# Kernel tuning notes

Measured on AMD Instinct MI355X. Metric: run time of the kernel, lower is better.

## Reference

```python
import jax, jax.numpy as jnp
import numpy as np

THRESHOLD = 0.3

def setup_inputs() -> dict:
    key = jax.random.key(0)
    ks = jax.random.split(key, 8)
    B, T, N, d = 4, 32, 1024, 2
    hd, od, hs, osz = 64, 64, 128, 2
    p = lambda k, sh: jax.random.normal(k, sh, jnp.float32) * 0.1
    return {
        "points": jax.random.uniform(ks[0], (B, T, N, d), jnp.float32),
        "W1": p(ks[1], (hd, d)),   "b1": jnp.zeros((hd,), jnp.float32),
        "W2": p(ks[2], (od, hd)),  "b2": jnp.zeros((od,), jnp.float32),
        "Wg": p(ks[3], (hd, od)),  "bg": jnp.zeros((hd,), jnp.float32),
        "Wih": p(ks[4], (3 * hs, hd)), "Whh": p(ks[5], (3 * hs, hs)),
        "bih": jnp.zeros((3 * hs,), jnp.float32), "bhh": jnp.zeros((3 * hs,), jnp.float32),
        "Wf": p(ks[6], (osz, hs)), "bf": jnp.zeros((osz,), jnp.float32),
    }

def _gcn_step(pts, W1, b1, W2, b2, Wg, bg):
    # pts: [N, d]. Torch detaches node features & adjacency (no grad to points).
    pts = jax.lax.stop_gradient(pts)
    dist = jnp.linalg.norm(pts[:, None, :] - pts[None, :, :], axis=2)  # [N,N]
    A = (dist < THRESHOLD).astype(pts.dtype)
    dinv = 1.0 / jnp.sqrt(A.sum(axis=1))          # rowsum >= 1 (self-loop)
    An = A * dinv[:, None] * dinv[None, :]        # D^{-1/2} A D^{-1/2}
    x = jax.nn.relu((An @ pts) @ W1.T + b1)       # [N, hd]
    x = jax.nn.relu((An @ x) @ W2.T + b2)         # [N, od]
    return x.mean(axis=0) @ Wg.T + bg             # [hd]

def reference(points, W1, b1, W2, b2, Wg, bg, Wih, Whh, bih, bhh, Wf, bf):
    # GCN per (batch, time): [B, T, hd]
    gcn = jax.vmap(jax.vmap(lambda p: _gcn_step(p, W1, b1, W2, b2, Wg, bg)))(points)
    H = Whh.shape[1]

    def gru_step(h, x):  # torch GRU gate order: r, z, n
        gi = x @ Wih.T + bih
        gh = h @ Whh.T + bhh
        ir, iz, inn = jnp.split(gi, 3)
        hr, hz, hn = jnp.split(gh, 3)
        r = jax.nn.sigmoid(ir + hr)
        z = jax.nn.sigmoid(iz + hz)
        n = jnp.tanh(inn + r * hn)
        h_new = (1.0 - z) * n + z * h
        return h_new, h_new

    h0 = jnp.zeros((H,), points.dtype)
    run = lambda xs: jax.lax.scan(gru_step, h0, xs)[1]   # [T, H]
    hs = jax.vmap(run)(gcn)                              # [B, T, H]
    y = hs @ Wf.T + bf                                   # [B, T, out]
    # torch: per-element gru_out.mean(dim=1, keepdim=True) on [1,T,out] -> [1,1,out], stacked -> [B,1,1,out]
    return y.mean(axis=1, keepdims=True)[:, :, None, :]
```

## Files before the change

kernel.cpp:

```cpp
#include <hip/hip_runtime.h>
#include <hip/hip_bf16.h>
#include <math.h>

#define N_PTS 1024
#define BT    128
typedef unsigned int u32;
typedef __attribute__((ext_vector_type(8))) short short8_t;
typedef __attribute__((ext_vector_type(4))) float f32x4;

__device__ __forceinline__ float bfi(u32 bits16) {
    union { u32 u; float f; } v; v.u = bits16 << 16; return v.f;
}
__device__ __forceinline__ unsigned short f2bf(float f) {
    union { float f; u32 u; } v; v.f = f;
    return (unsigned short)((v.u + 0x7FFFu + ((v.u >> 16) & 1u)) >> 16);
}
__device__ __forceinline__ float ldf(const void* p, int i, bool bf) {
    return bf ? bfi(((const unsigned short*)p)[i]) : ((const float*)p)[i];
}
__device__ __forceinline__ float2 ldp(const void* pbase, int j, bool bf) {
    if (bf) {
        u32 w = ((const u32*)pbase)[j];
        return make_float2(bfi(w & 0xFFFFu), bfi(w >> 16));
    }
    return ((const float2*)pbase)[j];
}
__device__ __forceinline__ bool detect_bf16(const void* pts, int tid, int* s_flag) {
    if (tid < 64) {
        u32 w = ((const u32*)pts)[tid];
        float v = bfi(w & 0xFFFFu);
        bool ok = (v >= 0.0f) && (v <= 1.0f);
        unsigned long long m = __ballot(ok);
        if (tid == 0) *s_flag = (m == 0xFFFFFFFFFFFFFFFFull) ? 1 : 0;
    }
    __syncthreads();
    return *s_flag != 0;
}
__device__ __forceinline__ bool is_nb(float px, float py, float qx, float qy) {
    float dx = px - qx, dy = py - qy;
    float d2 = __fadd_rn(__fmul_rn(dx, dx), __fmul_rn(dy, dy));
    return d2 < 0.09f;
}
__device__ __forceinline__ const void* pts_base(const void* pts, int bt, bool bf) {
    return bf ? (const void*)((const unsigned short*)pts + (size_t)bt * N_PTS * 2)
              : (const void*)((const float*)pts + (size_t)bt * N_PTS * 2);
}
__device__ __forceinline__ void gload16(const u32* g, u32* l) {
    __builtin_amdgcn_global_load_lds((const __attribute__((address_space(1))) u32*)g,
                                     (__attribute__((address_space(3))) u32*)l, 16, 0, 0);
}
__device__ __forceinline__ float rdlane(float v, int i) {
    return __int_as_float(__builtin_amdgcn_readlane(__float_as_int(v), i));
}

__global__ __launch_bounds__(256) void k1_bm(const void* __restrict__ pts,
                                             float* __restrict__ dinv,
                                             float* __restrict__ gsum,
                                             u32* __restrict__ bm) {
    int blk = blockIdx.x, tid = threadIdx.x;
    int bt = blk >> 2, q = blk & 3;
    __shared__ float2 sp[N_PTS];
    __shared__ int s_flag;
    bool bf = detect_bf16(pts, tid, &s_flag);
    const void* pb = pts_base(pts, bt, bf);
    for (int j = tid; j < N_PTS; j += 256) sp[j] = ldp(pb, j, bf);
    if (blk < 32) gsum[blk * 256 + tid] = 0.0f;
    __syncthreads();
    int i = q * 256 + tid;
    float px = sp[i].x, py = sp[i].y;
    const float4* sp4 = (const float4*)sp;
    u32* bmrow = bm + (size_t)bt * 32768 + i;
    int cnt = 0;
    for (int c = 0; c < 32; c++) {
        u32 m = 0;
#pragma unroll
        for (int h = 0; h < 8; h++) {
            float4 s01 = sp4[c * 16 + 2 * h], s23 = sp4[c * 16 + 2 * h + 1];
            if (is_nb(px, py, s01.x, s01.y)) m |= 1u << (4 * h);
            if (is_nb(px, py, s01.z, s01.w)) m |= 1u << (4 * h + 1);
            if (is_nb(px, py, s23.x, s23.y)) m |= 1u << (4 * h + 2);
            if (is_nb(px, py, s23.z, s23.w)) m |= 1u << (4 * h + 3);
        }
        bmrow[c * 1024] = m;
        cnt += __popc(m);
    }
    dinv[bt * N_PTS + i] = 1.0f / sqrtf((float)cnt);
}

__global__ __launch_bounds__(256) void k2_x1v(const void* __restrict__ pts,
                                              const void* __restrict__ W1,
                                              const void* __restrict__ b1,
                                              const float* __restrict__ dinv,
                                              const u32* __restrict__ bm,
                                              u32* __restrict__ x1vB) {
    int blk = blockIdx.x, tid = threadIdx.x;
    int bt = blk >> 2, q = blk & 3;
    __shared__ float2 sud[N_PTS];
    __shared__ float2 sax[256];
    __shared__ float  sdl[256];
    __shared__ int s_flag;
    bool bf = detect_bf16(pts, tid, &s_flag);
    const void* pb = pts_base(pts, bt, bf);
    for (int j = tid; j < N_PTS; j += 256) {
        float2 p = ldp(pb, j, bf);
        float d = dinv[bt * N_PTS + j];
        sud[j] = make_float2(d * p.x, d * p.y);
    }
    __syncthreads();
    int i = q * 256 + tid;
    float ax = 0.f, ay = 0.f;
    const u32* bmr = bm + (size_t)bt * 32768 + i;
    for (int c = 0; c < 32; c++) {
        u32 m = bmr[c * 1024];
        const float4* uv = (const float4*)sud + c * 16;
#pragma unroll
        for (int h = 0; h < 16; h++) {
            float4 v = uv[h];
            bool b0 = (m >> (2 * h)) & 1u, b1_ = (m >> (2 * h + 1)) & 1u;
            ax += b0 ? v.x : 0.0f;  ay += b0 ? v.y : 0.0f;
            ax += b1_ ? v.z : 0.0f; ay += b1_ ? v.w : 0.0f;
        }
    }
    float di = dinv[bt * N_PTS + i];
    sax[tid] = make_float2(ax * di, ay * di);
    sdl[tid] = di;
    __syncthreads();
    int ch = tid & 63, wq = tid >> 6;
    float w0 = ldf(W1, 2 * ch, bf), w1v = ldf(W1, 2 * ch + 1, bf), bb = ldf(b1, ch, bf);
    for (int tt = 0; tt < 4; tt++) {
        u32 ow[8];
#pragma unroll
        for (int k2i = 0; k2i < 8; k2i++) {
            int lj = tt * 64 + wq * 16 + 2 * k2i;
            float2 a0 = sax[lj], a1 = sax[lj + 1];
            float v0 = sdl[lj]     * fmaxf(fmaf(w0, a0.x, fmaf(w1v, a0.y, bb)), 0.0f);
            float v1 = sdl[lj + 1] * fmaxf(fmaf(w0, a1.x, fmaf(w1v, a1.y, bb)), 0.0f);
            ow[k2i] = (u32)f2bf(v0) | ((u32)f2bf(v1) << 16);
        }
        u32* dst = x1vB + ((size_t)(bt * 16 + q * 4 + tt) * 64 + ch) * 36 + wq * 8;
        *(uint4*)dst = make_uint4(ow[0], ow[1], ow[2], ow[3]);
        *(uint4*)(dst + 4) = make_uint4(ow[4], ow[5], ow[6], ow[7]);
    }
}

__global__ __launch_bounds__(256) void k3_mfma(const void* __restrict__ pts,
                                               const void* __restrict__ W2,
                                               const void* __restrict__ b2,
                                               const float* __restrict__ dinv,
                                               const u32* __restrict__ bm,
                                               const u32* __restrict__ x1vB,
                                               float* __restrict__ gsum) {
    __shared__ u32 pool[15424];
    __shared__ int s_flag;
    float* poolf = (float*)pool;
    int tid = threadIdx.x, lane = tid & 63, w = tid >> 6;
    int l15 = lane & 15, quad = lane >> 4;
    int blk = blockIdx.x, bt = blk & 127, rowblk = blk >> 7;
    bool bf = detect_bf16(pts, tid, &s_flag);

    const u32* xg = x1vB + (size_t)bt * 36864;
    for (int it = w; it < 9; it += 4)
        gload16(xg + it * 256 + lane * 4, pool + 8192 + it * 256 + lane * 4);

    const u32* bg_ = bm + (size_t)bt * 32768 + rowblk * 256;
    for (int idx = tid; idx < 8192; idx += 256) {
        int c = idx >> 8, r = idx & 255;
        pool[idx] = bg_[c * 1024 + r];
    }
    unsigned short* W2B = (unsigned short*)(pool + 12800);
    for (int idx = tid; idx < 4096; idx += 256) {
        int o = idx >> 6, c = idx & 63;
        W2B[o * 72 + c] = f2bf(ldf(W2, idx, bf));
    }
    if (tid < 256) poolf[15104 + tid] = dinv[bt * N_PTS + rowblk * 256 + tid];
    if (tid < 64)  poolf[15360 + tid] = ldf(b2, tid, bf);

    f32x4 acc[4][4];
#pragma unroll
    for (int rf = 0; rf < 4; rf++)
#pragma unroll
        for (int nb = 0; nb < 4; nb++)
#pragma unroll
            for (int r = 0; r < 4; r++) acc[rf][nb][r] = 0.0f;

    for (int t = 0; t < 16; t++) {
        __syncthreads();
        if (t + 1 < 16) {
            u32* dst = pool + ((t & 1) ? 8192 : 10496);
            const u32* src = xg + (t + 1) * 2304;
            for (int it = w; it < 9; it += 4)
                gload16(src + it * 256 + lane * 4, dst + it * 256 + lane * 4);
        }
        const unsigned short* xf = (const unsigned short*)(pool + ((t & 1) ? 10496 : 8192));
#pragma unroll
        for (int ks = 0; ks < 2; ks++) {
            short8_t bq[4];
#pragma unroll
            for (int rf = 0; rf < 4; rf++) {
                u32 mw = pool[(2 * t + ks) * 256 + w * 64 + rf * 16 + l15];
                u32 by = (mw >> (quad * 8)) & 0xFFu;
                short8_t v;
#pragma unroll
                for (int i2 = 0; i2 < 8; i2++)
                    v[i2] = (by & (1u << i2)) ? (short)0x3F80 : (short)0;
                bq[rf] = v;
            }
#pragma unroll
            for (int nb = 0; nb < 4; nb++) {
                short8_t af = *(const short8_t*)(xf + (nb * 16 + l15) * 72 + ks * 32 + quad * 8);
#pragma unroll
                for (int rf = 0; rf < 4; rf++)
                    acc[rf][nb] = __builtin_amdgcn_mfma_f32_16x16x32_bf16(af, bq[rf], acc[rf][nb], 0, 0, 0);
            }
        }
    }
    __syncthreads();

    u32* dump = pool;
#pragma unroll
    for (int rf = 0; rf < 4; rf++) {
        int rn = w * 64 + rf * 16 + l15;
        float di = poolf[15104 + rn];
#pragma unroll
        for (int nb = 0; nb < 4; nb++) {
            u32 lo = (u32)f2bf(acc[rf][nb][0] * di) | ((u32)f2bf(acc[rf][nb][1] * di) << 16);
            u32 hi = (u32)f2bf(acc[rf][nb][2] * di) | ((u32)f2bf(acc[rf][nb][3] * di) << 16);
            u32* dst = dump + rn * 36 + nb * 8 + quad * 2;
            dst[0] = lo; dst[1] = hi;
        }
    }
    __syncthreads();
    f32x4 xacc[4][4];
#pragma unroll
    for (int ob = 0; ob < 4; ob++)
#pragma unroll
        for (int rf = 0; rf < 4; rf++)
#pragma unroll
            for (int r = 0; r < 4; r++) xacc[ob][rf][r] = 0.0f;
#pragma unroll
    for (int ks2 = 0; ks2 < 2; ks2++) {
        short8_t b2f[4];
#pragma unroll
        for (int rf = 0; rf < 4; rf++)
            b2f[rf] = *(const short8_t*)((const unsigned short*)dump +
                        (w * 64 + rf * 16 + l15) * 72 + ks2 * 32 + quad * 8);
#pragma unroll
        for (int ob = 0; ob < 4; ob++) {
            short8_t a2 = *(const short8_t*)(W2B + (ob * 16 + l15) * 72 + ks2 * 32 + quad * 8);
#pragma unroll
            for (int rf = 0; rf < 4; rf++)
                xacc[ob][rf] = __builtin_amdgcn_mfma_f32_16x16x32_bf16(a2, b2f[rf], xacc[ob][rf], 0, 0, 0);
        }
    }
#pragma unroll
    for (int ob = 0; ob < 4; ob++) {
#pragma unroll
        for (int r = 0; r < 4; r++) {
            int o = ob * 16 + quad * 4 + r;
            float bb = poolf[15360 + o];
            float s = 0.0f;
#pragma unroll
            for (int rf = 0; rf < 4; rf++) s += fmaxf(xacc[ob][rf][r] + bb, 0.0f);
            s += __shfl_down(s, 8, 16);
            s += __shfl_down(s, 4, 16);
            s += __shfl_down(s, 2, 16);
            s += __shfl_down(s, 1, 16);
            if (l15 == 0) atomicAdd(&gsum[bt * 64 + o], s);
        }
    }
}

__global__ __launch_bounds__(768, 1) void k4_all(const void* __restrict__ pts,
                                                 const void* __restrict__ Wg,
                                                 const void* __restrict__ bg,
                                                 const void* __restrict__ Wih,
                                                 const void* __restrict__ Whh,
                                                 const void* __restrict__ bih,
                                                 const void* __restrict__ bhh,
                                                 const void* __restrict__ Wf,
                                                 const void* __restrict__ bf_,
                                                 const float* __restrict__ gsum,
                                                 float* __restrict__ out) {
    int b = blockIdx.x, tid = threadIdx.x;
    __shared__ float s_gi[32 * 384];
    __shared__ float sWgT[64 * 65];
    __shared__ float s_gm[2048];
    __shared__ float s_x[2048];
    __shared__ float s_part[768];
    __shared__ float s_h[128];
    __shared__ int s_flag;
    bool bf = detect_bf16(pts, tid, &s_flag);
    for (int idx = tid; idx < 4096; idx += 768) {
        int o = idx >> 6, k = idx & 63;
        sWgT[k * 65 + o] = ldf(Wg, idx, bf);
    }
    for (int idx = tid; idx < 2048; idx += 768)
        s_gm[idx] = gsum[(size_t)b * 2048 + idx] * (1.0f / 1024.0f);
    if (tid < 128) s_h[tid] = 0.0f;
    __syncthreads();
    for (int idx = tid; idx < 2048; idx += 768) {
        int t = idx >> 6, c = idx & 63;
        float s0 = ldf(bg, c, bf), s1 = 0.f, s2 = 0.f, s3 = 0.f;
        const float* gm = s_gm + t * 64;
#pragma unroll
        for (int k = 0; k < 64; k += 4) {
            s0 = fmaf(sWgT[k * 65 + c],       gm[k],     s0);
            s1 = fmaf(sWgT[(k + 1) * 65 + c], gm[k + 1], s1);
            s2 = fmaf(sWgT[(k + 2) * 65 + c], gm[k + 2], s2);
            s3 = fmaf(sWgT[(k + 3) * 65 + c], gm[k + 3], s3);
        }
        s_x[idx] = (s0 + s1) + (s2 + s3);
    }
    __syncthreads();
    int hi = (tid >= 384) ? 1 : 0;
    int r = tid - hi * 384;
    int lane = tid & 63;
    {
        float wv[64];
        if (bf) {
#pragma unroll
            for (int k = 0; k < 64; k++) wv[k] = bfi(((const unsigned short*)Wih)[r * 64 + k]);
        } else {
            const float4* wr = (const float4*)Wih + r * 16;
#pragma unroll
            for (int qq = 0; qq < 16; qq++) {
                float4 v = wr[qq];
                wv[4*qq] = v.x; wv[4*qq+1] = v.y; wv[4*qq+2] = v.z; wv[4*qq+3] = v.w;
            }
        }
        float br = ldf(bih, r, bf);
        for (int t = hi; t < 32; t += 2) {
            float xv = s_x[t * 64 + lane];
            float s0 = br, s1 = 0.f, s2 = 0.f, s3 = 0.f;
#pragma unroll
            for (int k = 0; k < 64; k += 4) {
                s0 = fmaf(wv[k],     rdlane(xv, k),     s0);
                s1 = fmaf(wv[k + 1], rdlane(xv, k + 1), s1);
                s2 = fmaf(wv[k + 2], rdlane(xv, k + 2), s2);
                s3 = fmaf(wv[k + 3], rdlane(xv, k + 3), s3);
            }
            s_gi[t * 384 + r] = (s0 + s1) + (s2 + s3);
        }
    }
    float wh2[64];
    {
        int koff = hi * 64;
        if (bf) {
#pragma unroll
            for (int k = 0; k < 64; k++)
                wh2[k] = bfi(((const unsigned short*)Whh)[r * 128 + koff + k]);
        } else {
            const float4* wr = (const float4*)Whh + (r * 128 + koff) / 4;
#pragma unroll
            for (int qq = 0; qq < 16; qq++) {
                float4 v = wr[qq];
                wh2[4*qq] = v.x; wh2[4*qq+1] = v.y; wh2[4*qq+2] = v.z; wh2[4*qq+3] = v.w;
            }
        }
    }
    float bhr = hi ? 0.0f : ldf(bhh, r, bf);
    float h_reg = 0.0f, hsum = 0.0f;
    __syncthreads();

    for (int t = 0; t < 32; t++) {
        float hval = s_h[hi * 64 + lane];
        float s0 = bhr, s1 = 0.f, s2 = 0.f, s3 = 0.f;
#pragma unroll
        for (int k = 0; k < 64; k += 4) {
            s0 = fmaf(wh2[k],     rdlane(hval, k),     s0);
            s1 = fmaf(wh2[k + 1], rdlane(hval, k + 1), s1);
            s2 = fmaf(wh2[k + 2], rdlane(hval, k + 2), s2);
            s3 = fmaf(wh2[k + 3], rdlane(hval, k + 3), s3);
        }
        s_part[tid] = (s0 + s1) + (s2 + s3);
        __syncthreads();
        if (tid < 128) {
            int c = tid;
            float gr = s_gi[t * 384 + c]       + s_part[c]       + s_part[384 + c];
            float gz = s_gi[t * 384 + 128 + c] + s_part[128 + c] + s_part[512 + c];
            float gn = s_gi[t * 384 + 256 + c];
            float hn = s_part[256 + c] + s_part[640 + c];
            float rr = 1.0f / (1.0f + expf(-gr));
            float z  = 1.0f / (1.0f + expf(-gz));
            float n  = tanhf(fmaf(rr, hn, gn));
            float hnew = (1.0f - z) * n + z * h_reg;
            h_reg = hnew; hsum += hnew; s_h[c] = hnew;
        }
        __syncthreads();
    }
    if (tid < 128) {
        float hm = hsum * (1.0f / 32.0f);
        s_part[tid]       = ldf(Wf, tid, bf) * hm;
        s_part[128 + tid] = ldf(Wf, 128 + tid, bf) * hm;
    }
    __syncthreads();
    if (tid < 2) {
        float s = ldf(bf_, tid, bf);
        for (int k = 0; k < 128; k++) s += s_part[tid * 128 + k];
        out[b * 2 + tid] = s;
    }
}

extern "C" void kernel_launch(void* const* d_in, const int* in_sizes, int n_in,
                              void* d_out, int out_size, void* d_ws, size_t ws_size,
                              hipStream_t stream) {
    const void* pts = d_in[0];
    const void* W1  = d_in[1];
    const void* b1  = d_in[2];
    const void* W2  = d_in[3];
    const void* b2  = d_in[4];
    const void* Wg  = d_in[5];
    const void* bg  = d_in[6];
    const void* Wih = d_in[7];
    const void* Whh = d_in[8];
    const void* bih = d_in[9];
    const void* bhh = d_in[10];
    const void* Wf  = d_in[11];
    const void* bf_ = d_in[12];

    float* dinv = (float*)d_ws;
    float* gsum = dinv + (size_t)BT * N_PTS;
    u32*   bm   = (u32*)(gsum + BT * 64);
    u32*   x1vB = bm + (size_t)BT * 32768;

    k1_bm  <<<512, 256, 0, stream>>>(pts, dinv, gsum, bm);
    k2_x1v <<<512, 256, 0, stream>>>(pts, W1, b1, dinv, bm, x1vB);
    k3_mfma<<<512, 256, 0, stream>>>(pts, W2, b2, dinv, bm, x1vB, gsum);
    k4_all <<<4, 768, 0, stream>>>(pts, Wg, bg, Wih, Whh, bih, bhh, Wf, bf_,
                                   gsum, (float*)d_out);
}
```

Measured before the change: 239.2 us.

## Compute GRU gates redundantly per wave to drop one barrier per step

New measurement: 242.2 us. No clear change (+1.3%).

```diff
diff --git a/kernel.cpp b/kernel.cpp
--- a/kernel.cpp
+++ b/kernel.cpp
@@ -51,6 +51,13 @@
 }
 __device__ __forceinline__ float rdlane(float v, int i) {
     return __int_as_float(__builtin_amdgcn_readlane(__float_as_int(v), i));
+}
+__device__ __forceinline__ float sigm_f(float x) {
+    return __fdividef(1.0f, 1.0f + __expf(-x));
+}
+__device__ __forceinline__ float tanh_f(float x) {
+    float e = __expf(2.0f * x);
+    return 1.0f - __fdividef(2.0f, e + 1.0f);
 }
 
 __global__ __launch_bounds__(256) void k1_bm(const void* __restrict__ pts,
@@ -286,8 +293,8 @@
     __shared__ float sWgT[64 * 65];
     __shared__ float s_gm[2048];
     __shared__ float s_x[2048];
-    __shared__ float s_part[768];
-    __shared__ float s_h[128];
+    __shared__ float s_part[2][768];
+    __shared__ float s_hm[128];
     __shared__ int s_flag;
     bool bf = detect_bf16(pts, tid, &s_flag);
     for (int idx = tid; idx < 4096; idx += 768) {
@@ -296,7 +303,6 @@
     }
     for (int idx = tid; idx < 2048; idx += 768)
         s_gm[idx] = gsum[(size_t)b * 2048 + idx] * (1.0f / 1024.0f);
-    if (tid < 128) s_h[tid] = 0.0f;
     __syncthreads();
     for (int idx = tid; idx < 2048; idx += 768) {
         int t = idx >> 6, c = idx & 63;
@@ -359,11 +365,15 @@
         }
     }
     float bhr = hi ? 0.0f : ldf(bhh, r, bf);
-    float h_reg = 0.0f, hsum = 0.0f;
+    int c = hi * 64 + lane;
+    float hval = 0.0f;
+    float hsum = 0.0f;
     __syncthreads();
 
     for (int t = 0; t < 32; t++) {
-        float hval = s_h[hi * 64 + lane];
+        float gi_r = s_gi[t * 384 + c];
+        float gi_z = s_gi[t * 384 + 128 + c];
+        float gi_n = s_gi[t * 384 + 256 + c];
         float s0 = bhr, s1 = 0.f, s2 = 0.f, s3 = 0.f;
 #pragma unroll
         for (int k = 0; k < 64; k += 4) {
@@ -372,31 +382,30 @@
             s2 = fmaf(wh2[k + 2], rdlane(hval, k + 2), s2);
             s3 = fmaf(wh2[k + 3], rdlane(hval, k + 3), s3);
         }
-        s_part[tid] = (s0 + s1) + (s2 + s3);
+        s_part[t & 1][tid] = (s0 + s1) + (s2 + s3);
         __syncthreads();
-        if (tid < 128) {
-            int c = tid;
-            float gr = s_gi[t * 384 + c]       + s_part[c]       + s_part[384 + c];
-            float gz = s_gi[t * 384 + 128 + c] + s_part[128 + c] + s_part[512 + c];
-            float gn = s_gi[t * 384 + 256 + c];
-            float hn = s_part[256 + c] + s_part[640 + c];
-            float rr = 1.0f / (1.0f + expf(-gr));
-            float z  = 1.0f / (1.0f + expf(-gz));
-            float n  = tanhf(fmaf(rr, hn, gn));
-            float hnew = (1.0f - z) * n + z * h_reg;
-            h_reg = hnew; hsum += hnew; s_h[c] = hnew;
-        }
-        __syncthreads();
-    }
+        const float* P = s_part[t & 1];
+        float gr = gi_r + P[c]       + P[384 + c];
+        float gz = gi_z + P[128 + c] + P[512 + c];
+        float hn =        P[256 + c] + P[640 + c];
+        float rr = sigm_f(gr);
+        float z  = sigm_f(gz);
+        float n  = tanh_f(fmaf(rr, hn, gi_n));
+        hval = fmaf(z, hval - n, n);
+        hsum += hval;
+    }
+    if (tid < 64) s_hm[tid] = hsum * (1.0f / 32.0f);
+    else if (tid >= 384 && tid < 448) s_hm[64 + lane] = hsum * (1.0f / 32.0f);
+    __syncthreads();
     if (tid < 128) {
-        float hm = hsum * (1.0f / 32.0f);
-        s_part[tid]       = ldf(Wf, tid, bf) * hm;
-        s_part[128 + tid] = ldf(Wf, 128 + tid, bf) * hm;
+        float hm = s_hm[tid];
+        s_part[0][tid]       = ldf(Wf, tid, bf) * hm;
+        s_part[0][128 + tid] = ldf(Wf, 128 + tid, bf) * hm;
     }
     __syncthreads();
     if (tid < 2) {
         float s = ldf(bf_, tid, bf);
-        for (int k = 0; k < 128; k++) s += s_part[tid * 128 + k];
+        for (int k = 0; k < 128; k++) s += s_part[0][tid * 128 + k];
         out[b * 2 + tid] = s;
     }
 }
```
